# Kernel optimization log

Measured on AMD Instinct MI355X. Metric: run time of the kernel, lower is better.

The kernel has to match this reference:

```python
import jax, jax.numpy as jnp
import numpy as np
from jax import lax


def setup_inputs() -> dict:
    key = jax.random.key(0)
    k1, k2 = jax.random.split(key)
    B, T, D = 32, 4096, 256
    x = jax.random.normal(k1, (B, T, D), dtype=jnp.float32)
    logit_alpha = jax.random.normal(k2, (D,), dtype=jnp.float32)
    return {"x": x, "logit_alpha": logit_alpha}


def _ema_scan(x, alpha):
    # Linear recurrence y_t = a_t * y_{t-1} + b_t is associative; use a
    # log-depth parallel scan over T instead of a sequential loop.
    B, T, D = x.shape
    one_minus_alpha = 1.0 - alpha  # [D]
    # y_0 = x_0  ->  a_0 = 0, b_0 = x_0 ; for t>=1: a_t = alpha, b_t = (1-alpha)*x_t
    a = jnp.concatenate(
        [jnp.zeros((B, 1, D), x.dtype), jnp.broadcast_to(alpha, (B, T - 1, D))],
        axis=1,
    )
    b = jnp.concatenate([x[:, :1, :], one_minus_alpha * x[:, 1:, :]], axis=1)

    def combine(e1, e2):
        a1, b1 = e1
        a2, b2 = e2
        return a1 * a2, a2 * b1 + b2

    _, y = lax.associative_scan(combine, (a, b), axis=1)
    return y


def reference(x, logit_alpha):
    # x: [B, T, D]; per-feature alpha in (0,1)
    alpha = jax.nn.sigmoid(logit_alpha)  # [D]
    return _ema_scan(x, alpha)
```

## Files before the change

kernel.cpp:

```cpp
#include <hip/hip_runtime.h>

#define B_  32
#define T_  4096
#define D_  256
#define D4_ 64

typedef float f32x4 __attribute__((ext_vector_type(4)));

__device__ __forceinline__ f32x4 sigmoid4(f32x4 v) {
    f32x4 r;
    r[0] = 1.0f / (1.0f + expf(-v[0]));
    r[1] = 1.0f / (1.0f + expf(-v[1]));
    r[2] = 1.0f / (1.0f + expf(-v[2]));
    r[3] = 1.0f / (1.0f + expf(-v[3]));
    return r;
}

__global__ __launch_bounds__(256) void ema_carry(
    const f32x4* __restrict__ x, const f32x4* __restrict__ la,
    f32x4* __restrict__ E, int NC, int L) {
    const int wid  = threadIdx.x >> 6;
    const int lane = threadIdx.x & 63;
    const int g = blockIdx.x * 4 + wid;
    const int b = g / NC;
    const int c = g % NC;

    const f32x4 al = sigmoid4(la[lane]);
    const f32x4 om = 1.0f - al;

    size_t idx = ((size_t)b * T_ + (size_t)c * L) * D4_ + lane;
    f32x4 y = 0.0f;
    int i0 = 0;
    if (c == 0) {
        y = x[idx];
        idx += D4_;
        i0 = 1;
    }
    #pragma unroll 8
    for (int i = i0; i < L; ++i) {
        y = al * y + om * x[idx];
        idx += D4_;
    }
    E[(size_t)g * D4_ + lane] = y;
}

__global__ __launch_bounds__(256) void ema_apply(
    const f32x4* __restrict__ x, const f32x4* __restrict__ la,
    const f32x4* __restrict__ E, f32x4* __restrict__ yout,
    int NC, int L, int log2L) {
    const int wid  = threadIdx.x >> 6;
    const int lane = threadIdx.x & 63;
    const int g = blockIdx.x * 4 + wid;
    const int b = g / NC;
    const int c = g % NC;

    const f32x4 al = sigmoid4(la[lane]);
    const f32x4 om = 1.0f - al;

    f32x4 aL = al;
    for (int k = 0; k < log2L; ++k) aL = aL * aL;
    const f32x4 aL2 = aL * aL;
    const f32x4 aL4 = aL2 * aL2;

    const f32x4* Eb = E + (size_t)b * NC * D4_;
    f32x4 H = 0.0f;
    int j = 0;
    for (; j + 4 <= c; j += 4) {
        f32x4 e0 = Eb[(size_t)(j + 0) * D4_ + lane];
        f32x4 e1 = Eb[(size_t)(j + 1) * D4_ + lane];
        f32x4 e2 = Eb[(size_t)(j + 2) * D4_ + lane];
        f32x4 e3 = Eb[(size_t)(j + 3) * D4_ + lane];
        H = aL4 * H + (((e0 * aL + e1) * aL + e2) * aL + e3);
    }
    for (; j < c; ++j)
        H = aL * H + Eb[(size_t)j * D4_ + lane];

    size_t idx = ((size_t)b * T_ + (size_t)c * L) * D4_ + lane;
    f32x4 acc = H;
    int i0 = 0;
    if (c == 0) {
        acc = x[idx];
        __builtin_nontemporal_store(acc, &yout[idx]);
        idx += D4_;
        i0 = 1;
    }
    #pragma unroll 8
    for (int i = i0; i < L; ++i) {
        acc = al * acc + om * x[idx];
        __builtin_nontemporal_store(acc, &yout[idx]);
        idx += D4_;
    }
}

extern "C" void kernel_launch(void* const* d_in, const int* in_sizes, int n_in,
                              void* d_out, int out_size, void* d_ws, size_t ws_size,
                              hipStream_t stream) {
    const f32x4* x  = (const f32x4*)d_in[0];
    const f32x4* la = (const f32x4*)d_in[1];
    f32x4* out = (f32x4*)d_out;

    int NC = 64;
    while (NC > 1 && (size_t)B_ * NC * D_ * sizeof(float) > ws_size) NC >>= 1;
    const int L = T_ / NC;
    int log2L = 0;
    while ((1 << log2L) < L) ++log2L;

    f32x4* E = (f32x4*)d_ws;
    const int ntasks = B_ * NC;
    dim3 blk(256);
    dim3 grd(ntasks / 4);

    ema_carry<<<grd, blk, 0, stream>>>(x, la, E, NC, L);
    ema_apply<<<grd, blk, 0, stream>>>(x, la, E, out, NC, L, log2L);
}
```

Before: 71.99 us.

## Add middle carry-scan kernel and double chunk count

Adds a third kernel that scans the per-chunk carries once per batch, using four segments combined through shared memory. Each apply wave then loads a single precomputed prefix instead of re-reducing all earlier chunk carries, which removed quadratic redundant carry reads. NC is raised from 64 to 128, so there are more, shorter chunks and more waves to spread across the GPU. The cost is an extra kernel launch, a very small serial escan grid of 32 blocks, and dead leftover code with a zero-multiply lambda. The chunk-power exponent (aL^NCS) is computed by repeated squaring, which is only correct when NCS is a power of two.

```diff
diff --git a/kernel.cpp b/kernel.cpp
--- a/kernel.cpp
+++ b/kernel.cpp
@@ -44,10 +44,61 @@
     E[(size_t)g * D4_ + lane] = y;
 }
 
+__global__ __launch_bounds__(256) void ema_escan(
+    const f32x4* __restrict__ la, const f32x4* __restrict__ E,
+    f32x4* __restrict__ H, int NC, int log2L) {
+    __shared__ f32x4 s_A[4][64];
+
+    const int b    = blockIdx.x;
+    const int lane = threadIdx.x & 63;
+    const int seg  = threadIdx.x >> 6;
+    const int NCS  = NC >> 2;
+    const int c0   = seg * NCS;
+
+    const f32x4 al = sigmoid4(la[lane]);
+    f32x4 aL = al;
+    for (int k = 0; k < log2L; ++k) aL = aL * aL;
+
+    const f32x4* Eb = E + (size_t)b * NC * D4_;
+    f32x4* Hb       = H + (size_t)b * NC * D4_;
+
+    f32x4 s = 0.0f;
+    for (int i = 0; i < NCS; ++i)
+        s = aL * s + Eb[(size_t)(c0 + i) * D4_ + lane];
+    s_A[seg][lane] = s;
+    __syncthreads();
+
+    f32x4 X = 0.0f;
+    #pragma unroll
+    for (int j = 0; j < 3; ++j)
+        if (j < seg) X =  s_A[j][lane] + [&]{
+            f32x4 t = X;
+            return t; }() * 0.0f;
+    X = 0.0f;
+    {
+        f32x4 aLn = aL;
+        int n = NCS;
+        int lg = 0; while ((1 << lg) < n) ++lg;
+        f32x4 m = aL;
+        for (int k = 0; k < lg; ++k) m = m * m;
+        (void)aLn;
+        #pragma unroll
+        for (int j = 0; j < 3; ++j)
+            if (j < seg) X = m * X + s_A[j][lane];
+    }
+
+    f32x4 h = X;
+    for (int i = 0; i < NCS; ++i) {
+        size_t o = (size_t)(c0 + i) * D4_ + lane;
+        Hb[o] = h;
+        h = aL * h + Eb[o];
+    }
+}
+
 __global__ __launch_bounds__(256) void ema_apply(
     const f32x4* __restrict__ x, const f32x4* __restrict__ la,
-    const f32x4* __restrict__ E, f32x4* __restrict__ yout,
-    int NC, int L, int log2L) {
+    const f32x4* __restrict__ H, f32x4* __restrict__ yout,
+    int NC, int L) {
     const int wid  = threadIdx.x >> 6;
     const int lane = threadIdx.x & 63;
     const int g = blockIdx.x * 4 + wid;
@@ -57,26 +108,8 @@
     const f32x4 al = sigmoid4(la[lane]);
     const f32x4 om = 1.0f - al;
 
-    f32x4 aL = al;
-    for (int k = 0; k < log2L; ++k) aL = aL * aL;
-    const f32x4 aL2 = aL * aL;
-    const f32x4 aL4 = aL2 * aL2;
-
-    const f32x4* Eb = E + (size_t)b * NC * D4_;
-    f32x4 H = 0.0f;
-    int j = 0;
-    for (; j + 4 <= c; j += 4) {
-        f32x4 e0 = Eb[(size_t)(j + 0) * D4_ + lane];
-        f32x4 e1 = Eb[(size_t)(j + 1) * D4_ + lane];
-        f32x4 e2 = Eb[(size_t)(j + 2) * D4_ + lane];
-        f32x4 e3 = Eb[(size_t)(j + 3) * D4_ + lane];
-        H = aL4 * H + (((e0 * aL + e1) * aL + e2) * aL + e3);
-    }
-    for (; j < c; ++j)
-        H = aL * H + Eb[(size_t)j * D4_ + lane];
-
     size_t idx = ((size_t)b * T_ + (size_t)c * L) * D4_ + lane;
-    f32x4 acc = H;
+    f32x4 acc = H[(size_t)g * D4_ + lane];
     int i0 = 0;
     if (c == 0) {
         acc = x[idx];
@@ -99,17 +132,19 @@
     const f32x4* la = (const f32x4*)d_in[1];
     f32x4* out = (f32x4*)d_out;
 
-    int NC = 64;
-    while (NC > 1 && (size_t)B_ * NC * D_ * sizeof(float) > ws_size) NC >>= 1;
+    int NC = 128;
+    while (NC > 4 && 2 * (size_t)B_ * NC * D_ * sizeof(float) > ws_size) NC >>= 1;
     const int L = T_ / NC;
     int log2L = 0;
     while ((1 << log2L) < L) ++log2L;
 
     f32x4* E = (f32x4*)d_ws;
+    f32x4* H = E + (size_t)B_ * NC * D4_;
     const int ntasks = B_ * NC;
     dim3 blk(256);
     dim3 grd(ntasks / 4);
 
     ema_carry<<<grd, blk, 0, stream>>>(x, la, E, NC, L);
-    ema_apply<<<grd, blk, 0, stream>>>(x, la, E, out, NC, L, log2L);
+    ema_escan<<<B_, blk, 0, stream>>>(la, E, H, NC, log2L);
+    ema_apply<<<grd, blk, 0, stream>>>(x, la, H, out, NC, L);
 }
```

New measurement: 81.44 us. 13.1% more time.
